# Kernel tuning notes

Measured on AMD Instinct MI355X. Metric: run time of the kernel, lower is better.

Reference implementation:

```python
import jax, jax.numpy as jnp
import numpy as np

NSAMPLE = 16   # knn neighbors for cost volume
KCLUST = 8     # cluster size stand-in for custom_cluster_pc1 (min_count=8)
B, N, D = 2, 4096, 64


def _sqdist(src, dst):
    # src [B,N,C], dst [B,M,C] -> [B,N,M]
    d = (jnp.sum(src * src, -1)[:, :, None]
         + jnp.sum(dst * dst, -1)[:, None, :]
         - 2.0 * jnp.einsum('bnc,bmc->bnm', src, dst))
    return jnp.maximum(d, 0.0)


def _knn(k, xyz, new_xyz):
    return jax.lax.top_k(-_sqdist(new_xyz, xyz), k)[1]  # [B,S,k] indices of k smallest


def _group(points, idx):
    # points [B,M,C], idx [B,N,K] -> [B,N,K,C]
    b = jnp.arange(points.shape[0])[:, None, None]
    return points[b, idx]


def _weightnet(x, w1, b1, w2, b2, w3, b3):
    # x [B,N,K,3]; 1x1 conv stack == per-point MLP, relu
    h = jax.nn.relu(jnp.einsum('bnkc,cd->bnkd', x, w1) + b1)
    h = jax.nn.relu(jnp.einsum('bnkc,cd->bnkd', h, w2) + b2)
    return jax.nn.relu(jnp.einsum('bnkc,cd->bnkd', h, w3) + b3)


def _leaky(x):
    return jnp.where(x > 0, x, 0.1 * x)


def _forward(xyz1, xyz2, points1, points2, vel1, vel2, mask1, mask2,
             w_xyz, w_vel, w_points,
             mlp_w1, mlp_b1, mlp_w2, mlp_b2,
             wn1_w1, wn1_b1, wn1_w2, wn1_b2, wn1_w3, wn1_b3,
             wn2_w1, wn2_b1, wn2_w2, wn2_b2, wn2_w3, wn2_b3):
    xyz1t = jnp.transpose(xyz1, (0, 2, 1))      # [B,N1,3]
    xyz2t = jnp.transpose(xyz2, (0, 2, 1))      # [B,N2,3]
    p1t = jnp.transpose(points1, (0, 2, 1))     # [B,N1,D1]
    p2t = jnp.transpose(points2, (0, 2, 1))     # [B,N2,D2]

    # --- custom_cluster_pc1 stand-in: knn clusters of pc1 with its velocities ---
    idx_c = _knn(KCLUST, xyz1t, xyz1t)                     # [B,N,KC]
    cc = _group(xyz1t, idx_c)                              # [B,N,KC,3]
    cv = _group(vel1[..., None], idx_c)[..., 0]            # [B,N,KC]

    u = cc / jnp.linalg.norm(cc, axis=-1, keepdims=True)
    ATA = jnp.einsum('bnki,bnkj->bnij', u, u) + 1e-6 * jnp.eye(3, dtype=u.dtype)
    ATb = jnp.einsum('bnki,bnk->bni', u, cv)
    v_world = jnp.linalg.solve(ATA, ATb[..., None])[..., 0]  # [B,N,3]

    # --- feature-space knn between weighted (xyz, points) concatenations ---
    f1 = jnp.concatenate([w_xyz * xyz1t, w_points * p1t], axis=-1)
    f2 = jnp.concatenate([w_xyz * xyz2t, w_points * p2t], axis=-1)
    knn_idx = _knn(NSAMPLE, f2, f1)                        # [B,N1,K]

    neighbor_xyz = _group(xyz2t, knn_idx)                  # [B,N1,K,3]
    direction_xyz = neighbor_xyz - xyz1t[:, :, None, :]
    g2 = _group(p2t, knn_idx)                              # [B,N1,K,D2]
    g1 = jnp.broadcast_to(p1t[:, :, None, :], g2.shape[:3] + (p1t.shape[-1],))
    new_points = jnp.concatenate([g1, g2, direction_xyz], axis=-1)  # [B,N1,K,D1+D2+3]

    h = _leaky(jnp.einsum('bnkc,cd->bnkd', new_points, mlp_w1) + mlp_b1)
    h = _leaky(jnp.einsum('bnkc,cd->bnkd', h, mlp_w2) + mlp_b2)    # [B,N1,K,128]

    w = _weightnet(direction_xyz, wn1_w1, wn1_b1, wn1_w2, wn1_b2, wn1_w3, wn1_b3)
    point_to_patch = jnp.sum(w * h, axis=2)                # [B,N1,128]

    # --- second grouping in rigid-velocity space ---
    idx2 = _knn(NSAMPLE, v_world, v_world)
    nxyz1 = _group(xyz1t, idx2)
    dir2 = nxyz1 - xyz1t[:, :, None, :]
    w2 = _weightnet(dir2, wn2_w1, wn2_b1, wn2_w2, wn2_b2, wn2_w3, wn2_b3)
    gcost = _group(point_to_patch, idx2)                   # [B,N1,K,128]
    patch_to_patch = jnp.sum(w2 * gcost, axis=2)           # [B,N1,128]

    return jnp.transpose(patch_to_patch, (0, 2, 1)), v_world  # [B,128,N1], [B,N1,3]


def setup_inputs() -> dict:
    key = jax.random.key(0)
    ks = jax.random.split(key, 24)
    s = 0.05
    inp = {
        'xyz1': jax.random.normal(ks[0], (B, 3, N), jnp.float32),
        'xyz2': jax.random.normal(ks[1], (B, 3, N), jnp.float32),
        'points1': jax.random.normal(ks[2], (B, D, N), jnp.float32),
        'points2': jax.random.normal(ks[3], (B, D, N), jnp.float32),
        'vel1': jax.random.normal(ks[4], (B, N), jnp.float32),
        'vel2': jax.random.normal(ks[5], (B, N), jnp.float32),
        'mask1': jnp.ones((B, N), jnp.float32),
        'mask2': jnp.ones((B, N), jnp.float32),
        'w_xyz': jnp.float32(0.4), 'w_vel': jnp.float32(0.2), 'w_points': jnp.float32(0.4),
        'mlp_w1': jax.random.normal(ks[6], (2 * D + 3, 128), jnp.float32) * s,
        'mlp_b1': jnp.zeros((128,), jnp.float32),
        'mlp_w2': jax.random.normal(ks[7], (128, 128), jnp.float32) * s,
        'mlp_b2': jnp.zeros((128,), jnp.float32),
    }
    for tag, base in (('wn1', 8), ('wn2', 14)):
        inp[f'{tag}_w1'] = jax.random.normal(ks[base], (3, 8), jnp.float32) * s
        inp[f'{tag}_b1'] = jnp.zeros((8,), jnp.float32)
        inp[f'{tag}_w2'] = jax.random.normal(ks[base + 1], (8, 8), jnp.float32) * s
        inp[f'{tag}_b2'] = jnp.zeros((8,), jnp.float32)
        inp[f'{tag}_w3'] = jax.random.normal(ks[base + 2], (8, 128), jnp.float32) * s
        inp[f'{tag}_b3'] = jnp.zeros((128,), jnp.float32)
    return inp


def reference(xyz1, xyz2, points1, points2, vel1, vel2, mask1, mask2,
              w_xyz, w_vel, w_points,
              mlp_w1, mlp_b1, mlp_w2, mlp_b2,
              wn1_w1, wn1_b1, wn1_w2, wn1_b2, wn1_w3, wn1_b3,
              wn2_w1, wn2_b1, wn2_w2, wn2_b2, wn2_w3, wn2_b3):
    return _forward(xyz1, xyz2, points1, points2, vel1, vel2, mask1, mask2,
                    w_xyz, w_vel, w_points,
                    mlp_w1, mlp_b1, mlp_w2, mlp_b2,
                    wn1_w1, wn1_b1, wn1_w2, wn1_b2, wn1_w3, wn1_b3,
                    wn2_w1, wn2_b1, wn2_w2, wn2_b2, wn2_w3, wn2_b3)
```

## Files before the change

kernel.cpp:

```cpp
#include <hip/hip_runtime.h>

#define NPTS 4096
#define NQ   8192
#define DD   64
#define KNN  16
#define KC   8
#define NSEG3 32
#define NPSEG 32
#define KB96 96
#define FSTR 104
#define VOFF 1048576

#define ALWAYS_INLINE __attribute__((always_inline)) inline

typedef __attribute__((ext_vector_type(8))) short bf16x8;
typedef __attribute__((ext_vector_type(4))) float f32x4;

__device__ ALWAYS_INLINE float leakyf(float x) { return x > 0.f ? x : 0.1f * x; }

__device__ ALWAYS_INLINE unsigned short bf16rne(float f) {
  unsigned u = __float_as_uint(f);
  u = (u + 0x7FFFu + ((u >> 16) & 1u)) >> 16;
  return (unsigned short)u;
}

__device__ ALWAYS_INLINE float packdt(float d, unsigned tag12) {
  return __uint_as_float((__float_as_uint(d) & 0xFFFFF000u) | tag12);
}

#define TK8_FOREACH(M)  M(0) M(1) M(2) M(3) M(4) M(5) M(6) M(7)
#define TK16_FOREACH(M) M(0) M(1) M(2) M(3) M(4) M(5) M(6) M(7) \
                        M(8) M(9) M(10) M(11) M(12) M(13) M(14) M(15)

#define TK_DECL1(i) float tkd##i = 3.4e38f; int tki##i = 0;
#define TK_STEP1(i) { bool c = vd < tkd##i; float t_ = tkd##i; int u_ = tki##i; \
                      tkd##i = c ? vd : tkd##i; tki##i = c ? vi : tki##i; \
                      vd = c ? t_ : vd; vi = c ? u_ : vi; }
#define TK8_DECL  TK8_FOREACH(TK_DECL1)
#define TK8_INS(dexp, mexp)  { float vd = (dexp); int vi = (mexp); \
                               if (vd < tkd7)  { TK8_FOREACH(TK_STEP1) } }
#define TK8_RESET1(i) tkd##i = 3.4e38f; tki##i = 0;

#define PK_DECL1(i) float pk##i = __uint_as_float(0x7F7FFFFFu);
#define PK_STEP1(i) { float lo_ = fminf(pk##i, pv); pv = fmaxf(pk##i, pv); pk##i = lo_; }
#define PK16_DECL    TK16_FOREACH(PK_DECL1)
#define PK16_INS(ve) { float pv = (ve); TK16_FOREACH(PK_STEP1) }
#define PK_STORE1(i) pdq[i] = pk##i;
#define PK16_STORE   TK16_FOREACH(PK_STORE1)

__global__ __launch_bounds__(256) void k_prep(
    const float* __restrict__ xyz1, const float* __restrict__ xyz2,
    const float* __restrict__ pts1, const float* __restrict__ pts2,
    const float* __restrict__ w_xyz_p, const float* __restrict__ w_points_p,
    unsigned short* __restrict__ f1b, unsigned short* __restrict__ f2b,
    float* __restrict__ n1, float* __restrict__ n2a,
    float* __restrict__ p1t, float* __restrict__ p2t,
    float* __restrict__ x1t, float* __restrict__ x2t)
{
  int tgid = blockIdx.x * 256 + threadIdx.x;
  int cloud = tgid >> 13;
  int gid = tgid & (NQ - 1);
  int b = gid >> 12, n = gid & (NPTS - 1);
  float wx = w_xyz_p[0], wp = w_points_p[0];
  const float* xyz = cloud ? xyz2 : xyz1;
  const float* pts = cloud ? pts2 : pts1;
  unsigned short* fb = cloud ? f2b : f1b;
  float* nrm = cloud ? n2a : n1;
  float* pt  = cloud ? p2t : p1t;
  float* xt  = cloud ? x2t : x1t;
  const float* xb = xyz + (size_t)b * 3 * NPTS;
  float x = xb[n], y = xb[NPTS + n], z = xb[2 * NPTS + n];
  float nrm2 = fmaf(z, z, fmaf(y, y, x * x));
  float4 xv; xv.x = x; xv.y = y; xv.z = z; xv.w = nrm2;
  *(float4*)&xt[(size_t)gid * 4] = xv;
  float fx = wx * x, fy = wx * y, fz = wx * z;
  float acc = fmaf(fz, fz, fmaf(fy, fy, fx * fx));
  unsigned short* fr = fb + (size_t)gid * KB96;
  fr[0] = bf16rne(fx); fr[1] = bf16rne(fy); fr[2] = bf16rne(fz);
  const float* pb = pts + (size_t)b * DD * NPTS;
  float* pr = pt + (size_t)gid * DD;
  for (int c = 0; c < DD; ++c) {
    float v = pb[(size_t)c * NPTS + n];
    pr[c] = v;
    float fv = wp * v;
    fr[3 + c] = bf16rne(fv);
    acc = fmaf(fv, fv, acc);
  }
  for (int c = 67; c < KB96; ++c) fr[c] = 0;
  nrm[gid] = acc;
}

__global__ __launch_bounds__(256) void k_knn3(
    const float* __restrict__ x4, float* __restrict__ pd, int* __restrict__ pi)
{
  __shared__ __align__(16) float4 sc[128];
  int seg = blockIdx.y;
  int Q = blockIdx.x * 256 + threadIdx.x;
  int b = Q >> 12;
  float4 q = *(const float4*)&x4[(size_t)Q * 4];
  TK8_DECL
  int gbase = (b << 12) + seg * 128;
  if (threadIdx.x < 128)
    sc[threadIdx.x] = *(const float4*)&x4[(size_t)(gbase + threadIdx.x) * 4];
  __syncthreads();
  int m0 = seg * 128;
#pragma unroll
  for (int j = 0; j < 128; ++j) {
    float4 c = sc[j];
    float dot = fmaf(q.z, c.z, fmaf(q.y, c.y, q.x * c.x));
    float d = fmaxf(q.w + c.w - 2.f * dot, 0.f);
    TK8_INS(d, m0 + j)
  }
  float* pdq = pd + ((size_t)Q * NSEG3 + seg) * 8;
  int* piq = pi + ((size_t)Q * NSEG3 + seg) * 8;
#define ST8(i) pdq[i] = tkd##i; piq[i] = tki##i;
  TK8_FOREACH(ST8)
#undef ST8
}

__global__ __launch_bounds__(256) void k_knnv(
    const float* __restrict__ x4, float* __restrict__ pd)
{
  __shared__ __align__(16) float4 sc[128];
  int seg = blockIdx.y;
  int Q = blockIdx.x * 256 + threadIdx.x;
  int b = Q >> 12;
  float4 q = *(const float4*)&x4[(size_t)Q * 4];
  PK16_DECL
  int gbase = (b << 12) + seg * 128;
  if (threadIdx.x < 128)
    sc[threadIdx.x] = *(const float4*)&x4[(size_t)(gbase + threadIdx.x) * 4];
  __syncthreads();
#pragma unroll
  for (int j = 0; j < 128; ++j) {
    float4 c = sc[j];
    float dot = fmaf(q.z, c.z, fmaf(q.y, c.y, q.x * c.x));
    float d = fmaxf(q.w + c.w - 2.f * dot, 0.f);
    PK16_INS(packdt(d, ((unsigned)j << 5) | (unsigned)seg))
  }
  float* pdq = pd + ((size_t)Q * NPSEG + seg) * 16;
  PK16_STORE
}

__global__ __launch_bounds__(256) void k_rigid(
    const float* __restrict__ pd, const int* __restrict__ pi,
    const float* __restrict__ x4, const float* __restrict__ vel1,
    float* __restrict__ vout, float* __restrict__ v4out)
{
  __shared__ __align__(16) float s_d[64][33];
  __shared__ __align__(16) int   s_i[64][33];
  int tid = threadIdx.x;
  int ql = tid >> 2, part = tid & 3;
  int Q = blockIdx.x * 64 + ql;
  int b = Q >> 12;
  TK8_DECL
  {
    int s0 = part * 8;
    const float* pbase = pd + ((size_t)Q * NSEG3 + s0) * 8;
    const int* ibase = pi + ((size_t)Q * NSEG3 + s0) * 8;
#pragma unroll
    for (int s = 0; s < 8; ++s) {
#pragma unroll
      for (int j = 0; j < 8; ++j) TK8_INS(pbase[s * 8 + j], ibase[s * 8 + j])
    }
  }
#define STP(i) s_d[ql][part * 8 + i] = tkd##i; s_i[ql][part * 8 + i] = tki##i;
  TK8_FOREACH(STP)
#undef STP
  __syncthreads();
  if (part != 0) return;
  TK8_FOREACH(TK8_RESET1)
#pragma unroll
  for (int j = 0; j < 32; ++j) TK8_INS(s_d[ql][j], s_i[ql][j])
  int base = b << 12;
  double a00 = 0, a01 = 0, a02 = 0, a11 = 0, a12 = 0, a22 = 0;
  double r0 = 0, r1 = 0, r2 = 0;
#define RIG_ACC(i) { \
    float4 c = *(const float4*)&x4[(size_t)(base + tki##i) * 4]; \
    float nr = sqrtf(c.w); \
    float ux = c.x / nr, uy = c.y / nr, uz = c.z / nr; \
    float cv = vel1[base + tki##i]; \
    double dx = ux, dy = uy, dz = uz, dvv = cv; \
    a00 += dx * dx; a01 += dx * dy; a02 += dx * dz; \
    a11 += dy * dy; a12 += dy * dz; a22 += dz * dz; \
    r0 += dx * dvv; r1 += dy * dvv; r2 += dz * dvv; }
  TK8_FOREACH(RIG_ACC)
#undef RIG_ACC
  a00 += 1e-6; a11 += 1e-6; a22 += 1e-6;
  double c00 = a11 * a22 - a12 * a12;
  double c01 = a02 * a12 - a01 * a22;
  double c02 = a01 * a12 - a02 * a11;
  double c11 = a00 * a22 - a02 * a02;
  double c12 = a02 * a01 - a00 * a12;
  double c22 = a00 * a11 - a01 * a01;
  double det = a00 * c00 + a01 * c01 + a02 * c02;
  double inv = 1.0 / det;
  float vx = (float)((c00 * r0 + c01 * r1 + c02 * r2) * inv);
  float vy = (float)((c01 * r0 + c11 * r1 + c12 * r2) * inv);
  float vz = (float)((c02 * r0 + c12 * r1 + c22 * r2) * inv);
  vout[(size_t)Q * 3 + 0] = vx;
  vout[(size_t)Q * 3 + 1] = vy;
  vout[(size_t)Q * 3 + 2] = vz;
  float4 v; v.x = vx; v.y = vy; v.z = vz;
  v.w = fmaf(vz, vz, fmaf(vy, vy, vx * vx));
  *(float4*)&v4out[(size_t)Q * 4] = v;
}

__global__ __launch_bounds__(256) void k_knnf_mfma(
    const unsigned short* __restrict__ f1b, const unsigned short* __restrict__ f2b,
    const float* __restrict__ n1, const float* __restrict__ n2a,
    float* __restrict__ pd)
{
  __shared__ __align__(16) unsigned short sf1[16 * FSTR];
  __shared__ __align__(16) unsigned short sf2[64 * FSTR];
  __shared__ __align__(16) float sn1[16];
  __shared__ __align__(16) float sn2[64];
  __shared__ __align__(16) float sD[64][17];
  int tid = threadIdx.x;
  int w = tid >> 6, lane = tid & 63;
  int i15 = lane & 15, g = lane >> 4, kr0 = g * 8;
  int blockq = blockIdx.x * 16;
  int b = blockq >> 12;
  int seg = blockIdx.y;
  int gbase = (b << 12) + seg * 2048;
  {
    const float4* src = (const float4*)(f1b + (size_t)blockq * KB96);
    if (tid < 192) ((float4*)sf1)[tid + tid / 12] = src[tid];
    if (tid < 16) sn1[tid] = n1[blockq + tid];
  }
  __syncthreads();
  bf16x8 af0 = *(const bf16x8*)&sf1[i15 * FSTR + kr0];
  bf16x8 af1 = *(const bf16x8*)&sf1[i15 * FSTR + 32 + kr0];
  bf16x8 af2 = *(const bf16x8*)&sf1[i15 * FSTR + 64 + kr0];
  float nq0 = sn1[g * 4 + 0], nq1 = sn1[g * 4 + 1];
  float nq2 = sn1[g * 4 + 2], nq3 = sn1[g * 4 + 3];
  PK16_DECL
  int q_tk = tid & 15, p_tk = tid >> 4;
  for (int ch = 0; ch < 32; ++ch) {
    __syncthreads();
    {
      const float4* src = (const float4*)(f2b + (size_t)(gbase + ch * 64) * KB96);
      int i0 = tid, i1 = tid + 256, i2 = tid + 512;
      ((float4*)sf2)[i0 + i0 / 12] = src[i0];
      ((float4*)sf2)[i1 + i1 / 12] = src[i1];
      ((float4*)sf2)[i2 + i2 / 12] = src[i2];
      if (tid < 64) sn2[tid] = n2a[gbase + ch * 64 + tid];
    }
    __syncthreads();
    {
      int crow = w * 16 + i15;
      const unsigned short* c_ = &sf2[crow * FSTR + kr0];
      f32x4 acc = {0.f, 0.f, 0.f, 0.f};
      acc = __builtin_amdgcn_mfma_f32_16x16x32_bf16(af0, *(const bf16x8*)&c_[0],  acc, 0, 0, 0);
      acc = __builtin_amdgcn_mfma_f32_16x16x32_bf16(af1, *(const bf16x8*)&c_[32], acc, 0, 0, 0);
      acc = __builtin_amdgcn_mfma_f32_16x16x32_bf16(af2, *(const bf16x8*)&c_[64], acc, 0, 0, 0);
      float nn2 = sn2[crow];
      unsigned tag = (((unsigned)(ch * 4 + (crow & 3))) << 5) |
                     (unsigned)(seg * 16 + (crow >> 2));
      sD[crow][g * 4 + 0] = packdt(fmaxf(nq0 + nn2 - 2.f * acc[0], 0.f), tag);
      sD[crow][g * 4 + 1] = packdt(fmaxf(nq1 + nn2 - 2.f * acc[1], 0.f), tag);
      sD[crow][g * 4 + 2] = packdt(fmaxf(nq2 + nn2 - 2.f * acc[2], 0.f), tag);
      sD[crow][g * 4 + 3] = packdt(fmaxf(nq3 + nn2 - 2.f * acc[3], 0.f), tag);
    }
    __syncthreads();
#pragma unroll
    for (int j = 0; j < 4; ++j)
      PK16_INS(sD[p_tk * 4 + j][q_tk])
  }
  int pseg = seg * 16 + p_tk;
  float* pdq = pd + ((size_t)(blockq + q_tk) * NPSEG + pseg) * 16;
  PK16_STORE
}

template<int MODE>
__global__ __launch_bounds__(256) void k_mergepk(
    const float* __restrict__ pd, int* __restrict__ oidx)
{
  int Q = blockIdx.x * 256 + threadIdx.x;
  PK16_DECL
  for (int s = 0; s < NPSEG; ++s) {
    const float* pdq = pd + ((size_t)Q * NPSEG + s) * 16;
    for (int j = 0; j < 16; ++j) {
      float v = pdq[j];
      if (__all(!(v < pk15))) break;
      PK16_INS(v)
    }
  }
#define DEC(i) { unsigned u = __float_as_uint(pk##i); int m_; \
    unsigned ps = u & 31u, lo = (u >> 5) & 127u; \
    if (MODE == 0) m_ = (int)(((ps >> 4) << 11) + ((lo >> 2) << 6) + ((ps & 15u) << 2) + (lo & 3u)); \
    else m_ = (int)((ps << 7) + lo); \
    oidx[(size_t)Q * KNN + i] = m_; }
  TK16_FOREACH(DEC)
#undef DEC
}

#define PPB 8
__device__ ALWAYS_INLINE bf16x8 load_wfrag(const float* __restrict__ Wg,
                                           int kbase, int col, int kmax) {
  bf16x8 r;
#pragma unroll
  for (int j = 0; j < 8; ++j) {
    int k = kbase + j;
    float f = (k < kmax) ? Wg[(size_t)k * 128 + col] : 0.f;
    r[j] = (short)bf16rne(f);
  }
  return r;
}

__global__ __launch_bounds__(512) void k_mlp_mfma(
    const float* __restrict__ p1t, const float* __restrict__ p2t,
    const float* __restrict__ x1t, const float* __restrict__ x2t,
    const int* __restrict__ kidx,
    const float* __restrict__ W1, const float* __restrict__ B1v,
    const float* __restrict__ W2, const float* __restrict__ B2v,
    const float* __restrict__ wnw1, const float* __restrict__ wnb1,
    const float* __restrict__ wnw2, const float* __restrict__ wnb2,
    const float* __restrict__ wnw3, const float* __restrict__ wnb3,
    float* __restrict__ ptp)
{
  __shared__ __align__(16) unsigned short sA1[16 * 168];
  __shared__ __align__(16) unsigned short sH1[16 * 136];
  __shared__ __align__(16) float s_wv[16 * 128];
  __shared__ __align__(16) float s_c1[24];
  __shared__ __align__(16) float s_cb1[8];
  __shared__ __align__(16) float s_c2[64];
  __shared__ __align__(16) float s_cb2[8];
  __shared__ __align__(16) float s_w3[1024];
  __shared__ __align__(16) float s_b3[128];
  int tid = threadIdx.x;
  int w = tid >> 6, lane = tid & 63;
  int col = (w << 4) + (lane & 15);
  int kr0 = (lane >> 4) * 8;
  if (tid < 24) s_c1[tid] = wnw1[tid];
  else if (tid < 32) s_cb1[tid - 24] = wnb1[tid - 24];
  else if (tid < 96) s_c2[tid - 32] = wnw2[tid - 32];
  else if (tid < 104) s_cb2[tid - 96] = wnb2[tid - 96];
  if (tid >= 128 && tid < 256) s_b3[tid - 128] = wnb3[tid - 128];
  for (int i = tid; i < 1024; i += 512) s_w3[i] = wnw3[i];
  bf16x8 w1f0 = load_wfrag(W1, 0 + kr0, col, 131);
  bf16x8 w1f1 = load_wfrag(W1, 32 + kr0, col, 131);
  bf16x8 w1f2 = load_wfrag(W1, 64 + kr0, col, 131);
  bf16x8 w1f3 = load_wfrag(W1, 96 + kr0, col, 131);
  bf16x8 w1f4 = load_wfrag(W1, 128 + kr0, col, 131);
  bf16x8 w2f0 = load_wfrag(W2, 0 + kr0, col, 128);
  bf16x8 w2f1 = load_wfrag(W2, 32 + kr0, col, 128);
  bf16x8 w2f2 = load_wfrag(W2, 64 + kr0, col, 128);
  bf16x8 w2f3 = load_wfrag(W2, 96 + kr0, col, 128);
  float b1c = B1v[col], b2c = B2v[col];
  int blk0 = blockIdx.x * PPB;
  int base = (blk0 >> 12) << 12;
  int r_st = tid >> 5, t_st = tid & 31;

  for (int p = 0; p < PPB; ++p) {
    int gid = blk0 + p;
    __syncthreads();
    {
      int m = kidx[(size_t)gid * 16 + r_st];
      int grow = base + m;
      float4 cx1 = *(const float4*)&x1t[(size_t)gid * 4];
      float4 cx2 = *(const float4*)&x2t[(size_t)grow * 4];
      unsigned short* row = &sA1[r_st * 168];
      row[t_st]      = bf16rne(p1t[(size_t)gid * 64 + t_st]);
      row[t_st + 32] = bf16rne(p1t[(size_t)gid * 64 + t_st + 32]);
      row[t_st + 64] = bf16rne(p2t[(size_t)grow * 64 + t_st]);
      row[t_st + 96] = bf16rne(p2t[(size_t)grow * 64 + t_st + 32]);
      float dx = cx2.x - cx1.x, dy = cx2.y - cx1.y, dz = cx2.z - cx1.z;
      float dv_ = (t_st == 0) ? dx : (t_st == 1) ? dy : (t_st == 2) ? dz : 0.f;
      row[t_st + 128] = bf16rne(dv_);
      float h1w0 = fmaxf(fmaf(dz, s_c1[16], fmaf(dy, s_c1[8],  fmaf(dx, s_c1[0], s_cb1[0]))), 0.f);
      float h1w1 = fmaxf(fmaf(dz, s_c1[17], fmaf(dy, s_c1[9],  fmaf(dx, s_c1[1], s_cb1[1]))), 0.f);
      float h1w2 = fmaxf(fmaf(dz, s_c1[18], fmaf(dy, s_c1[10], fmaf(dx, s_c1[2], s_cb1[2]))), 0.f);
      float h1w3 = fmaxf(fmaf(dz, s_c1[19], fmaf(dy, s_c1[11], fmaf(dx, s_c1[3], s_cb1[3]))), 0.f);
      float h1w4 = fmaxf(fmaf(dz, s_c1[20], fmaf(dy, s_c1[12], fmaf(dx, s_c1[4], s_cb1[4]))), 0.f);
      float h1w5 = fmaxf(fmaf(dz, s_c1[21], fmaf(dy, s_c1[13], fmaf(dx, s_c1[5], s_cb1[5]))), 0.f);
      float h1w6 = fmaxf(fmaf(dz, s_c1[22], fmaf(dy, s_c1[14], fmaf(dx, s_c1[6], s_cb1[6]))), 0.f);
      float h1w7 = fmaxf(fmaf(dz, s_c1[23], fmaf(dy, s_c1[15], fmaf(dx, s_c1[7], s_cb1[7]))), 0.f);
#define H2W(j) float h2w##j; { float a_ = s_cb2[j]; \
      a_ = fmaf(h1w0, s_c2[0 * 8 + j], a_); a_ = fmaf(h1w1, s_c2[1 * 8 + j], a_); \
      a_ = fmaf(h1w2, s_c2[2 * 8 + j], a_); a_ = fmaf(h1w3, s_c2[3 * 8 + j], a_); \
      a_ = fmaf(h1w4, s_c2[4 * 8 + j], a_); a_ = fmaf(h1w5, s_c2[5 * 8 + j], a_); \
      a_ = fmaf(h1w6, s_c2[6 * 8 + j], a_); a_ = fmaf(h1w7, s_c2[7 * 8 + j], a_); \
      h2w##j = fmaxf(a_, 0.f); }
      H2W(0) H2W(1) H2W(2) H2W(3) H2W(4) H2W(5) H2W(6) H2W(7)
#undef H2W
      int c4 = t_st * 4;
      float4 wv = *(const float4*)&s_b3[c4];
#define WV(j) { float4 w3 = *(const float4*)&s_w3[j * 128 + c4]; \
      wv.x = fmaf(h2w##j, w3.x, wv.x); wv.y = fmaf(h2w##j, w3.y, wv.y); \
      wv.z = fmaf(h2w##j, w3.z, wv.z); wv.w = fmaf(h2w##j, w3.w, wv.w); }
      WV(0) WV(1) WV(2) WV(3) WV(4) WV(5) WV(6) WV(7)
#undef WV
      wv.x = fmaxf(wv.x, 0.f); wv.y = fmaxf(wv.y, 0.f);
      wv.z = fmaxf(wv.z, 0.f); wv.w = fmaxf(wv.w, 0.f);
      *(float4*)&s_wv[r_st * 128 + c4] = wv;
    }
    __syncthreads();
    {
      int ab = (lane & 15) * 168 + kr0;
      f32x4 acc = {0.f, 0.f, 0.f, 0.f};
      acc = __builtin_amdgcn_mfma_f32_16x16x32_bf16(*(const bf16x8*)&sA1[ab],       w1f0, acc, 0, 0, 0);
      acc = __builtin_amdgcn_mfma_f32_16x16x32_bf16(*(const bf16x8*)&sA1[ab + 32],  w1f1, acc, 0, 0, 0);
      acc = __builtin_amdgcn_mfma_f32_16x16x32_bf16(*(const bf16x8*)&sA1[ab + 64],  w1f2, acc, 0, 0, 0);
      acc = __builtin_amdgcn_mfma_f32_16x16x32_bf16(*(const bf16x8*)&sA1[ab + 96],  w1f3, acc, 0, 0, 0);
      acc = __builtin_amdgcn_mfma_f32_16x16x32_bf16(*(const bf16x8*)&sA1[ab + 128], w1f4, acc, 0, 0, 0);
      int rw0 = (lane >> 4) * 4;
#pragma unroll
      for (int r = 0; r < 4; ++r)
        sH1[(rw0 + r) * 136 + col] = bf16rne(leakyf(acc[r] + b1c));
    }
    __syncthreads();
    {
      int ab = (lane & 15) * 136 + kr0;
      f32x4 acc = {0.f, 0.f, 0.f, 0.f};
      acc = __builtin_amdgcn_mfma_f32_16x16x32_bf16(*(const bf16x8*)&sH1[ab],      w2f0, acc, 0, 0, 0);
      acc = __builtin_amdgcn_mfma_f32_16x16x32_bf16(*(const bf16x8*)&sH1[ab + 32], w2f1, acc, 0, 0, 0);
      acc = __builtin_amdgcn_mfma_f32_16x16x32_bf16(*(const bf16x8*)&sH1[ab + 64], w2f2, acc, 0, 0, 0);
      acc = __builtin_amdgcn_mfma_f32_16x16x32_bf16(*(const bf16x8*)&sH1[ab + 96], w2f3, acc, 0, 0, 0);
      int rw0 = (lane >> 4) * 4;
      float v = 0.f;
#pragma unroll
      for (int r = 0; r < 4; ++r)
        v = fmaf(s_wv[(rw0 + r) * 128 + col], leakyf(acc[r] + b2c), v);
      v += __shfl_xor(v, 16);
      v += __shfl_xor(v, 32);
      if (lane < 16) ptp[(size_t)gid * 128 + col] = v;
    }
  }
}

__global__ __launch_bounds__(256) void k_final(
    const float* __restrict__ x1t, const int* __restrict__ idx2,
    const float* __restrict__ ptp,
    const float* __restrict__ wnw1, const float* __restrict__ wnb1,
    const float* __restrict__ wnw2, const float* __restrict__ wnb2,
    const float* __restrict__ wnw3, const float* __restrict__ wnb3,
    float* __restrict__ out0)
{
  __shared__ __align__(16) float s_gc[16][128];
  __shared__ __align__(16) float s_wn[16][8];
  __shared__ __align__(16) float s_red[2][128];
  int gid = blockIdx.x, b = gid >> 12, n = gid & (NPTS - 1);
  int tid = threadIdx.x;
  if (tid < 16) {
    int m = idx2[(size_t)gid * 16 + tid];
    float4 c2 = *(const float4*)&x1t[(size_t)((b << 12) + m) * 4];
    float4 c1 = *(const float4*)&x1t[(size_t)gid * 4];
    float dx = c2.x - c1.x, dy = c2.y - c1.y, dz = c2.z - c1.z;
    float h1w[8];
#pragma unroll
    for (int j = 0; j < 8; ++j)
      h1w[j] = fmaxf(fmaf(dz, wnw1[16 + j], fmaf(dy, wnw1[8 + j], fmaf(dx, wnw1[j], wnb1[j]))), 0.f);
#pragma unroll
    for (int j = 0; j < 8; ++j) {
      float a = wnb2[j];
#pragma unroll
      for (int qq = 0; qq < 8; ++qq) a = fmaf(h1w[qq], wnw2[qq * 8 + j], a);
      s_wn[tid][j] = fmaxf(a, 0.f);
    }
  }
  int k2 = tid >> 4, i2 = tid & 15;
  int mg = idx2[(size_t)gid * 16 + k2];
  const float* src = &ptp[(size_t)((b << 12) + mg) * 128 + i2 * 8];
  *(float4*)&s_gc[k2][i2 * 8] = *(const float4*)&src[0];
  *(float4*)&s_gc[k2][i2 * 8 + 4] = *(const float4*)&src[4];
  __syncthreads();
  int ch = tid & 127, kg2 = tid >> 7;
  float r = 0.f;
#pragma unroll
  for (int jj = 0; jj < 8; ++jj) {
    int k = kg2 * 8 + jj;
    float4 wa = *(const float4*)&s_wn[k][0];
    float4 wb = *(const float4*)&s_wn[k][4];
    float wv = wnb3[ch];
    wv = fmaf(wa.x, wnw3[ch], wv);
    wv = fmaf(wa.y, wnw3[128 + ch], wv);
    wv = fmaf(wa.z, wnw3[256 + ch], wv);
    wv = fmaf(wa.w, wnw3[384 + ch], wv);
    wv = fmaf(wb.x, wnw3[512 + ch], wv);
    wv = fmaf(wb.y, wnw3[640 + ch], wv);
    wv = fmaf(wb.z, wnw3[768 + ch], wv);
    wv = fmaf(wb.w, wnw3[896 + ch], wv);
    wv = fmaxf(wv, 0.f);
    r = fmaf(wv, s_gc[k][ch], r);
  }
  s_red[kg2][ch] = r;
  __syncthreads();
  if (tid < 128)
    out0[(size_t)(b * 128 + tid) * NPTS + n] = s_red[0][tid] + s_red[1][tid];
}

extern "C" void kernel_launch(void* const* d_in, const int* in_sizes, int n_in,
                              void* d_out, int out_size, void* d_ws, size_t ws_size,
                              hipStream_t stream) {
  (void)in_sizes; (void)n_in; (void)out_size; (void)ws_size;
  const float* xyz1   = (const float*)d_in[0];
  const float* xyz2   = (const float*)d_in[1];
  const float* pts1   = (const float*)d_in[2];
  const float* pts2   = (const float*)d_in[3];
  const float* vel1   = (const float*)d_in[4];
  const float* w_xyz  = (const float*)d_in[8];
  const float* w_pts  = (const float*)d_in[10];
  const float* mlp_w1 = (const float*)d_in[11];
  const float* mlp_b1 = (const float*)d_in[12];
  const float* mlp_w2 = (const float*)d_in[13];
  const float* mlp_b2 = (const float*)d_in[14];
  const float* wn1_w1 = (const float*)d_in[15];
  const float* wn1_b1 = (const float*)d_in[16];
  const float* wn1_w2 = (const float*)d_in[17];
  const float* wn1_b2 = (const float*)d_in[18];
  const float* wn1_w3 = (const float*)d_in[19];
  const float* wn1_b3 = (const float*)d_in[20];
  const float* wn2_w1 = (const float*)d_in[21];
  const float* wn2_b1 = (const float*)d_in[22];
  const float* wn2_w2 = (const float*)d_in[23];
  const float* wn2_b2 = (const float*)d_in[24];
  const float* wn2_w3 = (const float*)d_in[25];
  const float* wn2_b3 = (const float*)d_in[26];

  char* ws = (char*)d_ws;
  size_t off = 0;
  float* pd   = (float*)(ws + off); off += (size_t)NQ * NPSEG * 16 * 4;
  int*   pi   = (int*)(ws + off);   off += (size_t)NQ * NSEG3 * 8 * 4;
  unsigned short* f1b = (unsigned short*)(ws + off); off += (size_t)NQ * KB96 * 2;
  unsigned short* f2b = (unsigned short*)(ws + off); off += (size_t)NQ * KB96 * 2;
  float* n1   = (float*)(ws + off); off += (size_t)NQ * 4;
  float* n2a  = (float*)(ws + off); off += (size_t)NQ * 4;
  float* p1t  = (float*)(ws + off); off += (size_t)NQ * DD * 4;
  float* p2t  = (float*)(ws + off); off += (size_t)NQ * DD * 4;
  float* x1t  = (float*)(ws + off); off += (size_t)NQ * 4 * 4;
  float* x2t  = (float*)(ws + off); off += (size_t)NQ * 4 * 4;
  int*   kidx = (int*)(ws + off);   off += (size_t)NQ * KNN * 4;
  float* ptp  = (float*)(ws + off); off += (size_t)NQ * 128 * 4;
  int*   idx2 = (int*)(ws + off);   off += (size_t)NQ * KNN * 4;
  float* v4   = (float*)(ws + off); off += (size_t)NQ * 4 * 4;

  float* out0 = (float*)d_out;
  float* outv = (float*)d_out + VOFF;

  k_prep<<<64, 256, 0, stream>>>(xyz1, xyz2, pts1, pts2, w_xyz, w_pts,
                                 f1b, f2b, n1, n2a, p1t, p2t, x1t, x2t);
  k_knn3<<<dim3(32, NSEG3), 256, 0, stream>>>(x1t, pd, pi);
  k_rigid<<<128, 256, 0, stream>>>(pd, pi, x1t, vel1, outv, v4);
  k_knnf_mfma<<<dim3(NQ / 16, 2), 256, 0, stream>>>(f1b, f2b, n1, n2a, pd);
  k_mergepk<0><<<32, 256, 0, stream>>>(pd, kidx);
  k_mlp_mfma<<<NQ / PPB, 512, 0, stream>>>(p1t, p2t, x1t, x2t, kidx,
                                           mlp_w1, mlp_b1, mlp_w2, mlp_b2,
                                           wn1_w1, wn1_b1, wn1_w2, wn1_b2,
                                           wn1_w3, wn1_b3, ptp);
  k_knnv<<<dim3(32, 32), 256, 0, stream>>>(v4, pd);
  k_mergepk<1><<<32, 256, 0, stream>>>(pd, idx2);
  k_final<<<NQ, 256, 0, stream>>>(x1t, idx2, ptp,
                                  wn2_w1, wn2_b1, wn2_w2, wn2_b2, wn2_w3, wn2_b3, out0);
}
```

Baseline: 386.0 us.

## Double-buffer feature tiles in knn kernel and split merge across four threads per query

The feature-space kNN kernel now double-buffers the candidate tile in shared memory. The next chunk's global loads are issued before the partial top-k insertion on the current chunk, so load latency overlaps with compute, at the cost of doubling the sf2/sn2 shared memory. The merge kernel now gives each query four threads, each merging 8 segments; the four partial top-16 lists are then combined through shared memory by one thread. This raises the merge grid from 32 to 128 blocks and replaces the wave-wide early break with a per-thread break.

```diff
diff --git a/kernel.cpp b/kernel.cpp
--- a/kernel.cpp
+++ b/kernel.cpp
@@ -42,6 +42,7 @@
 #define TK8_RESET1(i) tkd##i = 3.4e38f; tki##i = 0;
 
 #define PK_DECL1(i) float pk##i = __uint_as_float(0x7F7FFFFFu);
+#define PK_RESET1(i) pk##i = __uint_as_float(0x7F7FFFFFu);
 #define PK_STEP1(i) { float lo_ = fminf(pk##i, pv); pv = fmaxf(pk##i, pv); pk##i = lo_; }
 #define PK16_DECL    TK16_FOREACH(PK_DECL1)
 #define PK16_INS(ve) { float pv = (ve); TK16_FOREACH(PK_STEP1) }
@@ -212,9 +213,9 @@
     float* __restrict__ pd)
 {
   __shared__ __align__(16) unsigned short sf1[16 * FSTR];
-  __shared__ __align__(16) unsigned short sf2[64 * FSTR];
+  __shared__ __align__(16) unsigned short sf2[2][64 * FSTR];
   __shared__ __align__(16) float sn1[16];
-  __shared__ __align__(16) float sn2[64];
+  __shared__ __align__(16) float sn2[2][64];
   __shared__ __align__(16) float sD[64][17];
   int tid = threadIdx.x;
   int w = tid >> 6, lane = tid & 63;
@@ -228,6 +229,14 @@
     if (tid < 192) ((float4*)sf1)[tid + tid / 12] = src[tid];
     if (tid < 16) sn1[tid] = n1[blockq + tid];
   }
+  {
+    const float4* src = (const float4*)(f2b + (size_t)gbase * KB96);
+    int i0 = tid, i1 = tid + 256, i2 = tid + 512;
+    ((float4*)sf2[0])[i0 + i0 / 12] = src[i0];
+    ((float4*)sf2[0])[i1 + i1 / 12] = src[i1];
+    ((float4*)sf2[0])[i2 + i2 / 12] = src[i2];
+    if (tid < 64) sn2[0][tid] = n2a[gbase + tid];
+  }
   __syncthreads();
   bf16x8 af0 = *(const bf16x8*)&sf1[i15 * FSTR + kr0];
   bf16x8 af1 = *(const bf16x8*)&sf1[i15 * FSTR + 32 + kr0];
@@ -237,24 +246,15 @@
   PK16_DECL
   int q_tk = tid & 15, p_tk = tid >> 4;
   for (int ch = 0; ch < 32; ++ch) {
-    __syncthreads();
-    {
-      const float4* src = (const float4*)(f2b + (size_t)(gbase + ch * 64) * KB96);
-      int i0 = tid, i1 = tid + 256, i2 = tid + 512;
-      ((float4*)sf2)[i0 + i0 / 12] = src[i0];
-      ((float4*)sf2)[i1 + i1 / 12] = src[i1];
-      ((float4*)sf2)[i2 + i2 / 12] = src[i2];
-      if (tid < 64) sn2[tid] = n2a[gbase + ch * 64 + tid];
-    }
-    __syncthreads();
+    int cur = ch & 1;
     {
       int crow = w * 16 + i15;
-      const unsigned short* c_ = &sf2[crow * FSTR + kr0];
+      const unsigned short* c_ = &sf2[cur][crow * FSTR + kr0];
       f32x4 acc = {0.f, 0.f, 0.f, 0.f};
       acc = __builtin_amdgcn_mfma_f32_16x16x32_bf16(af0, *(const bf16x8*)&c_[0],  acc, 0, 0, 0);
       acc = __builtin_amdgcn_mfma_f32_16x16x32_bf16(af1, *(const bf16x8*)&c_[32], acc, 0, 0, 0);
       acc = __builtin_amdgcn_mfma_f32_16x16x32_bf16(af2, *(const bf16x8*)&c_[64], acc, 0, 0, 0);
-      float nn2 = sn2[crow];
+      float nn2 = sn2[cur][crow];
       unsigned tag = (((unsigned)(ch * 4 + (crow & 3))) << 5) |
                      (unsigned)(seg * 16 + (crow >> 2));
       sD[crow][g * 4 + 0] = packdt(fmaxf(nq0 + nn2 - 2.f * acc[0], 0.f), tag);
@@ -263,9 +263,18 @@
       sD[crow][g * 4 + 3] = packdt(fmaxf(nq3 + nn2 - 2.f * acc[3], 0.f), tag);
     }
     __syncthreads();
+    if (ch + 1 < 32) {
+      const float4* src = (const float4*)(f2b + (size_t)(gbase + (ch + 1) * 64) * KB96);
+      int i0 = tid, i1 = tid + 256, i2 = tid + 512;
+      ((float4*)sf2[cur ^ 1])[i0 + i0 / 12] = src[i0];
+      ((float4*)sf2[cur ^ 1])[i1 + i1 / 12] = src[i1];
+      ((float4*)sf2[cur ^ 1])[i2 + i2 / 12] = src[i2];
+      if (tid < 64) sn2[cur ^ 1][tid] = n2a[gbase + (ch + 1) * 64 + tid];
+    }
 #pragma unroll
     for (int j = 0; j < 4; ++j)
       PK16_INS(sD[p_tk * 4 + j][q_tk])
+    __syncthreads();
   }
   int pseg = seg * 16 + p_tk;
   float* pdq = pd + ((size_t)(blockq + q_tk) * NPSEG + pseg) * 16;
@@ -276,13 +285,33 @@
 __global__ __launch_bounds__(256) void k_mergepk(
     const float* __restrict__ pd, int* __restrict__ oidx)
 {
-  int Q = blockIdx.x * 256 + threadIdx.x;
+  __shared__ __align__(16) float s_k[64][65];
+  int tid = threadIdx.x;
+  int ql = tid >> 2, part = tid & 3;
+  int Q = blockIdx.x * 64 + ql;
   PK16_DECL
-  for (int s = 0; s < NPSEG; ++s) {
-    const float* pdq = pd + ((size_t)Q * NPSEG + s) * 16;
+  {
+    const float* pbase = pd + ((size_t)Q * NPSEG + part * 8) * 16;
+#pragma unroll
+    for (int s = 0; s < 8; ++s) {
+      for (int j = 0; j < 16; ++j) {
+        float v = pbase[s * 16 + j];
+        if (!(v < pk15)) break;
+        PK16_INS(v)
+      }
+    }
+  }
+#define STK(i) s_k[ql][part * 16 + i] = pk##i;
+  TK16_FOREACH(STK)
+#undef STK
+  __syncthreads();
+  if (part != 0) return;
+  TK16_FOREACH(PK_RESET1)
+#pragma unroll
+  for (int p = 0; p < 4; ++p) {
     for (int j = 0; j < 16; ++j) {
-      float v = pdq[j];
-      if (__all(!(v < pk15))) break;
+      float v = s_k[ql][p * 16 + j];
+      if (!(v < pk15)) break;
       PK16_INS(v)
     }
   }
@@ -543,13 +572,13 @@
   k_knn3<<<dim3(32, NSEG3), 256, 0, stream>>>(x1t, pd, pi);
   k_rigid<<<128, 256, 0, stream>>>(pd, pi, x1t, vel1, outv, v4);
   k_knnf_mfma<<<dim3(NQ / 16, 2), 256, 0, stream>>>(f1b, f2b, n1, n2a, pd);
-  k_mergepk<0><<<32, 256, 0, stream>>>(pd, kidx);
+  k_mergepk<0><<<128, 256, 0, stream>>>(pd, kidx);
   k_mlp_mfma<<<NQ / PPB, 512, 0, stream>>>(p1t, p2t, x1t, x2t, kidx,
                                            mlp_w1, mlp_b1, mlp_w2, mlp_b2,
                                            wn1_w1, wn1_b1, wn1_w2, wn1_b2,
                                            wn1_w3, wn1_b3, ptp);
   k_knnv<<<dim3(32, 32), 256, 0, stream>>>(v4, pd);
-  k_mergepk<1><<<32, 256, 0, stream>>>(pd, idx2);
+  k_mergepk<1><<<128, 256, 0, stream>>>(pd, idx2);
   k_final<<<NQ, 256, 0, stream>>>(x1t, idx2, ptp,
                                   wn2_w1, wn2_b1, wn2_w2, wn2_b2, wn2_w3, wn2_b3, out0);
 }
```

Result: faster. 347.4 us (-10.0%).
